# Kernel optimization log

Measured on AMD Instinct MI355X. Metric: run time of the kernel, lower is better.

The kernel has to match this reference:

```python
import jax, jax.numpy as jnp
import numpy as np

B, N, IN, HID, OUT = 64, 256, 7, 64, 32
DEG = 32
NT = B * N          # total nodes per side
E = NT * DEG        # intra-graph edges per side
TAU = 1.0
MAX_ITER = 10
EPS = 1e-5          # InstanceNorm2d eps


def setup_inputs() -> dict:
    key = jax.random.key(0)
    ks = jax.random.split(key, 12)

    def edges(k):
        # random intra-graph edges: local indices in [0, N) plus per-graph offset
        loc = jax.random.randint(k, (2, B, N * DEG), 0, N)
        off = (jnp.arange(B) * N)[None, :, None]
        return (loc + off).reshape(2, -1).astype(jnp.int64)

    def lin(k, fi, fo):
        return jax.random.normal(k, (fi, fo), jnp.float32) / np.float32(np.sqrt(fi))

    return {
        "x1": jax.random.normal(ks[0], (NT, IN), jnp.float32),
        "x2": jax.random.normal(ks[1], (NT, IN), jnp.float32),
        "edge1": edges(ks[2]),
        "edge2": edges(ks[3]),
        "Wl1": lin(ks[4], IN, HID), "Wr1": lin(ks[5], IN, HID),
        "bl1": jnp.zeros((HID,), jnp.float32), "br1": jnp.zeros((HID,), jnp.float32),
        "att1": jax.random.normal(ks[6], (HID,), jnp.float32) * 0.1,
        "bias1": jnp.zeros((HID,), jnp.float32),
        "Wl2": lin(ks[7], HID, OUT), "Wr2": lin(ks[8], HID, OUT),
        "bl2": jnp.zeros((OUT,), jnp.float32), "br2": jnp.zeros((OUT,), jnp.float32),
        "att2": jax.random.normal(ks[9], (OUT,), jnp.float32) * 0.1,
        "bias2": jnp.zeros((OUT,), jnp.float32),
        "gamma": jnp.ones((1,), jnp.float32),
        "beta": jnp.zeros((1,), jnp.float32),
    }


def _gatv2(x, src, dst, Wl, bl, Wr, br, att, bias):
    # PyG GATv2Conv, heads=1: score = att . leaky_relu(lin_l(x_j) + lin_r(x_i))
    xl = x @ Wl + bl  # source transform
    xr = x @ Wr + br  # target transform
    e = jax.nn.leaky_relu(xl[src] + xr[dst], 0.2)     # [E, D]
    score = e @ att                                    # [E]
    smax = jax.ops.segment_max(score, dst, num_segments=NT)
    ex = jnp.exp(score - smax[dst])
    den = jax.ops.segment_sum(ex, dst, num_segments=NT)
    alpha = ex / den[dst]
    out = jax.ops.segment_sum(alpha[:, None] * xl[src], dst, num_segments=NT)
    return out + bias


def _encode(x, edge, params):
    # add self loops (PyG add_self_loops=True default)
    loops = jnp.arange(NT)
    src = jnp.concatenate([edge[0], loops])
    dst = jnp.concatenate([edge[1], loops])
    h = jax.nn.relu(_gatv2(x, src, dst, *params[0]))
    return _gatv2(h, src, dst, *params[1])


def _soft_topk(sim_n):
    # AFAT-style differentiable top-k: OT between flattened scores and
    # {min, max} anchors with marginals [(n-k)/n, k/n], k = N2 per pair.
    n = N * N
    k = N
    flat = sim_n.reshape(B, n)
    mn = flat.min(axis=1, keepdims=True)
    mx = flat.max(axis=1, keepdims=True)
    dist = jnp.stack([flat - mn, mx - flat], axis=-1)  # [B, n, 2] (|s-min|,|s-max|)
    logK = -dist / TAU
    log_row = -jnp.log(jnp.float32(n))
    log_col = jnp.log(jnp.array([(n - k) / n, k / n], jnp.float32))
    for i in range(MAX_ITER):
        if i % 2 == 0:  # row normalization to uniform 1/n
            logK = logK - jax.scipy.special.logsumexp(logK, axis=-1, keepdims=True) + log_row
        else:           # column normalization to [(n-k)/n, k/n]
            logK = logK - jax.scipy.special.logsumexp(logK, axis=1, keepdims=True) + log_col[None, None, :]
    soft = jnp.clip(jnp.exp(logK[:, :, 1]) * n, 0.0, 1.0)  # selection probability per entry
    return soft.reshape(B, N, N)


def reference(x1, x2, edge1, edge2, Wl1, Wr1, bl1, br1, att1, bias1,
              Wl2, Wr2, bl2, br2, att2, bias2, gamma, beta):
    params = ((Wl1, bl1, Wr1, br1, att1, bias1), (Wl2, bl2, Wr2, br2, att2, bias2))
    h1 = _encode(x1, edge1, params).reshape(B, N, OUT)
    h2 = _encode(x2, edge2, params).reshape(B, N, OUT)
    sim = jnp.einsum('bnd,bmd->bnm', h1, h2)
    # InstanceNorm2d(1, affine=True): normalize each pair's sim matrix
    mu = sim.mean(axis=(1, 2), keepdims=True)
    var = sim.var(axis=(1, 2), keepdims=True)
    sim_n = gamma[0] * (sim - mu) * jax.lax.rsqrt(var + EPS) + beta[0]
    return _soft_topk(sim_n)  # soft_S stacked over the batch, [B, N, N]
```

## Files before the change

kernel.cpp:

```cpp
#include <hip/hip_runtime.h>

#define NB 64
#define NN 256
#define IND 7
#define HIDD 64
#define OUTD 32
#define EPG 8192
#define ETOT 524288
#define CAPQ 2600
#define SRCPAD 2624

typedef _Float16 f16;
typedef f16 f16x2 __attribute__((ext_vector_type(2)));
typedef f16 f16x4 __attribute__((ext_vector_type(4)));
typedef f16 f16x8 __attribute__((ext_vector_type(8)));
typedef float f32x4 __attribute__((ext_vector_type(4)));

__device__ __forceinline__ float bsum16(float v, float* rb){
#pragma unroll
  for (int o = 32; o > 0; o >>= 1) v += __shfl_xor(v, o, 64);
  __syncthreads();
  if ((threadIdx.x & 63) == 0) rb[threadIdx.x >> 6] = v;
  __syncthreads();
  float s = 0.f;
#pragma unroll
  for (int i = 0; i < 16; i++) s += rb[i];
  return s;
}

__device__ __forceinline__ f16x2 lrelu2(f16x2 s){
  const f16x2 k = {(f16)0.2f, (f16)0.2f};
  return __builtin_elementwise_max(s, s * k);
}
__device__ __forceinline__ f16x2 shfl_h2(f16x2 v, int lane){
  int i = __builtin_bit_cast(int, v);
  i = __shfl(i, lane, 64);
  return __builtin_bit_cast(f16x2, i);
}

__global__ __launch_bounds__(512, 4) void gat1(
    const float* __restrict__ x1, const float* __restrict__ x2,
    const int* __restrict__ e1, const int* __restrict__ e2,
    const float* __restrict__ Wl, const float* __restrict__ Wr,
    const float* __restrict__ bl, const float* __restrict__ br,
    const float* __restrict__ att, const float* __restrict__ bias,
    f16* __restrict__ hmid,
    int* __restrict__ meta, unsigned char* __restrict__ srcs)
{
  __shared__ __align__(16) f16 xl_s[256 * 72];
  __shared__ float sc_s[CAPQ + 8];
  __shared__ unsigned int src_su[SRCPAD / 4];
  __shared__ int deg_s[64], start_s[64], cnt_s[64];
  __shared__ unsigned char perm[64];
  unsigned char* src_s = (unsigned char*)src_su;

  const int bid = blockIdx.x;
  const int gs = bid & 127, lo = (bid >> 7) * 64;
  const int side = gs >> 6, g = gs & 63;
  const float* x = side ? x2 : x1;
  const int* eb = side ? e2 : e1;
  const int* es = eb + g * EPG;
  const int* ed = eb + ETOT + g * EPG;
  const int t = threadIdx.x;

  if (t < 64) deg_s[t] = 0;

  unsigned short epk[17];
  int nE = 0;
#pragma unroll
  for (int i = 0; i < 17; i++){
    int e = t + i * 512;
    if (e < EPG + 256){
      int sl, dl;
      if (e < EPG){ sl = es[e] & 255; dl = ed[e] & 255; }
      else { sl = dl = e - EPG; }
      epk[i] = (unsigned short)((dl << 8) | sl);
      nE = i + 1;
    }
  }

  {
    const int node = t >> 1, dh = t & 1;
    float xv[IND];
    const float* xr_ = x + (g * 256 + node) * IND;
#pragma unroll
    for (int k = 0; k < IND; k++) xv[k] = xr_[k];
#pragma unroll
    for (int ch = 0; ch < 4; ch++){
      f16x8 o;
#pragma unroll
      for (int j = 0; j < 8; j++){
        int dd = dh * 32 + ch * 8 + j;
        float a = bl[dd];
#pragma unroll
        for (int k = 0; k < IND; k++) a = fmaf(xv[k], Wl[k * HIDD + dd], a);
        o[j] = (f16)a;
      }
      *(f16x8*)&xl_s[node * 72 + dh * 32 + ch * 8] = o;
    }
  }
  __syncthreads();

#pragma unroll
  for (int i = 0; i < 17; i++) if (i < nE){
    int r = (epk[i] >> 8) - lo;
    if ((unsigned)r < 64u) atomicAdd(&deg_s[r], 1);
  }
  __syncthreads();
  if (t < 64){
    int v = deg_s[t], s = v;
#pragma unroll
    for (int off = 1; off < 64; off <<= 1){
      int u = __shfl_up(s, off, 64);
      if (t >= off) s += u;
    }
    start_s[t] = s - v;
    cnt_s[t] = s - v;
    meta[bid * 128 + t] = s - v;
    meta[bid * 128 + 64 + t] = v;
    int r = 0;
#pragma unroll 8
    for (int j = 0; j < 64; j++){
      int dj = deg_s[j];
      r += (dj < v) || (dj == v && j < t);
    }
    perm[r] = (unsigned char)t;
  }
  __syncthreads();
#pragma unroll
  for (int i = 0; i < 17; i++) if (i < nE){
    int dl = epk[i] >> 8, r = dl - lo;
    if ((unsigned)r < 64u){
      int p = atomicAdd(&cnt_s[r], 1);
      if (p < CAPQ) src_s[p] = (unsigned char)(epk[i] & 255);
    }
  }
  __syncthreads();
  {
    int ttl = start_s[63] + deg_s[63];
    if (ttl > CAPQ) ttl = CAPQ;
    unsigned int* gsrc = (unsigned int*)(srcs + (size_t)bid * SRCPAD);
    int nw = (ttl + 3) >> 2;
    for (int i = t; i < nw; i += 512) gsrc[i] = src_su[i];
  }

  const int pairi = perm[t >> 3], sub = t & 7, ln = lo + pairi;
  f16x2 m[4], am[4];
  {
    float xv[IND];
    const float* xq = x + (g * 256 + ln) * IND;
#pragma unroll
    for (int k = 0; k < IND; k++) xv[k] = xq[k];
#pragma unroll
    for (int c = 0; c < 4; c++){
#pragma unroll
      for (int u = 0; u < 2; u++){
        int dd = sub * 8 + 2 * c + u;
        float a = br[dd];
#pragma unroll
        for (int k = 0; k < IND; k++) a = fmaf(xv[k], Wr[k * HIDD + dd], a);
        m[c][u] = (f16)a;
        am[c][u] = (f16)att[dd];
      }
    }
  }
  f16x2 xrh[32], atth[32];
  {
    const int base = (t & 63) & ~7;
#pragma unroll
    for (int ss = 0; ss < 8; ss++){
#pragma unroll
      for (int c = 0; c < 4; c++){
        xrh[ss * 4 + c] = shfl_h2(m[c], base + ss);
        atth[ss * 4 + c] = shfl_h2(am[c], base + ss);
      }
    }
  }

  const int s0 = start_s[pairi];
  int sE = s0 + deg_s[pairi];
  if (sE > CAPQ) sE = CAPQ;
  float ssum = 0.f;
  for (int idx = s0 + sub; idx < sE; idx += 8){
    int sl = src_s[idx];
    const f16x8* rp = (const f16x8*)&xl_s[(unsigned)sl * 72];
    float accs[4] = {0.f, 0.f, 0.f, 0.f};
#pragma unroll
    for (int blk = 0; blk < 8; blk++){
      f16x8 rv = rp[blk];
#pragma unroll
      for (int u = 0; u < 4; u++){
        f16x2 v = {rv[2 * u], rv[2 * u + 1]};
        v = v + xrh[blk * 4 + u];
        accs[u] = __builtin_amdgcn_fdot2(lrelu2(v), atth[blk * 4 + u], accs[u], false);
      }
    }
    float w = __expf((accs[0] + accs[1]) + (accs[2] + accs[3]));
    sc_s[idx] = w;
    ssum += w;
  }
  ssum += __shfl_xor(ssum, 1, 64);
  ssum += __shfl_xor(ssum, 2, 64);
  ssum += __shfl_xor(ssum, 4, 64);
  float inv = 1.f / ssum;
  float acc[8];
#pragma unroll
  for (int c = 0; c < 8; c++) acc[c] = 0.f;
  for (int base = s0; base < sE; base += 4){
    f16x8 rows[4]; float wv[4];
#pragma unroll
    for (int k = 0; k < 4; k++){
      int sl = src_s[base + k];
      rows[k] = *(const f16x8*)&xl_s[(unsigned)sl * 72 + sub * 8];
      wv[k] = sc_s[base + k];
    }
#pragma unroll
    for (int k = 0; k < 4; k++){
      float w = (base + k < sE) ? wv[k] : 0.f;
#pragma unroll
      for (int c = 0; c < 8; c++) acc[c] = fmaf(w, (float)rows[k][c], acc[c]);
    }
  }
  f16x8 o;
#pragma unroll
  for (int c = 0; c < 8; c++)
    o[c] = (f16)fmaxf(acc[c] * inv + bias[sub * 8 + c], 0.f);
  *(f16x8*)(hmid + (size_t)(gs * 256 + ln) * 64 + sub * 8) = o;
}

__global__ __launch_bounds__(512, 4) void gat2(
    const int* __restrict__ meta, const unsigned char* __restrict__ srcs,
    const f16* __restrict__ hmid,
    const float* __restrict__ Wl, const float* __restrict__ Wr,
    const float* __restrict__ bl, const float* __restrict__ br,
    const float* __restrict__ att, const float* __restrict__ bias,
    f16* __restrict__ hout)
{
  __shared__ __align__(16) f16 xl_s[256 * 40];
  __shared__ __align__(16) f16 xr_s[64 * 40];
  __shared__ float sc_s[CAPQ + 8];
  __shared__ unsigned int src_su[SRCPAD / 4];
  __shared__ int start_s[64], deg_s[64];
  __shared__ unsigned char perm[64];
  unsigned char* src_s = (unsigned char*)src_su;

  const int bid = blockIdx.x;
  const int gs = bid & 127, lo = (bid >> 7) * 64;
  const int t = threadIdx.x;

  if (t < 64){
    start_s[t] = meta[bid * 128 + t];
    deg_s[t] = meta[bid * 128 + 64 + t];
  }
  {
    int ttl = meta[bid * 128 + 63] + meta[bid * 128 + 64 + 63];
    if (ttl > CAPQ) ttl = CAPQ;
    const unsigned int* gsrc = (const unsigned int*)(srcs + (size_t)bid * SRCPAD);
    int nw = (ttl + 3) >> 2;
    for (int i = t; i < nw; i += 512) src_su[i] = gsrc[i];
  }

  {
    const int w = t >> 6, lane = t & 63;
    const int m = lane & 15, quad = lane >> 4;
    f16x8 a[2][2];
#pragma unroll
    for (int ti = 0; ti < 2; ti++){
      const f16* arow = hmid + (size_t)(gs * 256 + (2 * w + ti) * 16 + m) * 64;
      a[ti][0] = *(const f16x8*)(arow + quad * 8);
      a[ti][1] = *(const f16x8*)(arow + 32 + quad * 8);
    }
#pragma unroll
    for (int H = 0; H < 2; H++){
      const int n = H * 16 + m;
      f16x8 b0, b1;
#pragma unroll
      for (int j = 0; j < 8; j++){
        b0[j] = (f16)Wl[(quad * 8 + j) * 32 + n];
        b1[j] = (f16)Wl[(32 + quad * 8 + j) * 32 + n];
      }
      const float bv = bl[n];
#pragma unroll
      for (int ti = 0; ti < 2; ti++){
        f32x4 acc = {0.f, 0.f, 0.f, 0.f};
        acc = __builtin_amdgcn_mfma_f32_16x16x32_f16(a[ti][0], b0, acc, 0, 0, 0);
        acc = __builtin_amdgcn_mfma_f32_16x16x32_f16(a[ti][1], b1, acc, 0, 0, 0);
#pragma unroll
        for (int r = 0; r < 4; r++)
          xl_s[((2 * w + ti) * 16 + quad * 4 + r) * 40 + n] = (f16)(acc[r] + bv);
      }
    }
    if (w < 4){
      const f16* arow = hmid + (size_t)(gs * 256 + lo + w * 16 + m) * 64;
      f16x8 c0 = *(const f16x8*)(arow + quad * 8);
      f16x8 c1 = *(const f16x8*)(arow + 32 + quad * 8);
#pragma unroll
      for (int H = 0; H < 2; H++){
        const int n = H * 16 + m;
        f16x8 b0, b1;
#pragma unroll
        for (int j = 0; j < 8; j++){
          b0[j] = (f16)Wr[(quad * 8 + j) * 32 + n];
          b1[j] = (f16)Wr[(32 + quad * 8 + j) * 32 + n];
        }
        const float bv = br[n];
        f32x4 acc = {0.f, 0.f, 0.f, 0.f};
        acc = __builtin_amdgcn_mfma_f32_16x16x32_f16(c0, b0, acc, 0, 0, 0);
        acc = __builtin_amdgcn_mfma_f32_16x16x32_f16(c1, b1, acc, 0, 0, 0);
#pragma unroll
        for (int r = 0; r < 4; r++)
          xr_s[(w * 16 + quad * 4 + r) * 40 + n] = (f16)(acc[r] + bv);
      }
    }
  }
  __syncthreads();
  if (t < 64){
    int v = deg_s[t], r = 0;
#pragma unroll 8
    for (int j = 0; j < 64; j++){
      int dj = deg_s[j];
      r += (dj < v) || (dj == v && j < t);
    }
    perm[r] = (unsigned char)t;
  }
  __syncthreads();

  const int pairi = perm[t >> 3], sub = t & 7, ln = lo + pairi;
  f16x2 xrh[16], atth[16];
  {
    const f16x8* xrp = (const f16x8*)&xr_s[pairi * 40];
#pragma unroll
    for (int q = 0; q < 4; q++){
      f16x8 v = xrp[q];
#pragma unroll
      for (int u = 0; u < 4; u++){
        xrh[q * 4 + u][0] = v[2 * u];
        xrh[q * 4 + u][1] = v[2 * u + 1];
      }
    }
#pragma unroll
    for (int i = 0; i < 16; i++){
      atth[i][0] = (f16)att[2 * i];
      atth[i][1] = (f16)att[2 * i + 1];
    }
  }

  const int s0 = start_s[pairi];
  int sE = s0 + deg_s[pairi];
  if (sE > CAPQ) sE = CAPQ;
  float ssum = 0.f;
  for (int idx = s0 + sub; idx < sE; idx += 8){
    int sl = src_s[idx];
    const f16x8* rp = (const f16x8*)&xl_s[(unsigned)sl * 40];
    float accs[4] = {0.f, 0.f, 0.f, 0.f};
#pragma unroll
    for (int blk = 0; blk < 4; blk++){
      f16x8 rv = rp[blk];
#pragma unroll
      for (int u = 0; u < 4; u++){
        f16x2 v = {rv[2 * u], rv[2 * u + 1]};
        v = v + xrh[blk * 4 + u];
        accs[u] = __builtin_amdgcn_fdot2(lrelu2(v), atth[blk * 4 + u], accs[u], false);
      }
    }
    float w = __expf((accs[0] + accs[1]) + (accs[2] + accs[3]));
    sc_s[idx] = w;
    ssum += w;
  }
  ssum += __shfl_xor(ssum, 1, 64);
  ssum += __shfl_xor(ssum, 2, 64);
  ssum += __shfl_xor(ssum, 4, 64);
  float inv = 1.f / ssum;

  float acc[4];
#pragma unroll
  for (int c = 0; c < 4; c++) acc[c] = 0.f;
  for (int base = s0; base < sE; base += 8){
    f16x4 rows[8]; float wv[8];
#pragma unroll
    for (int k = 0; k < 8; k++){
      int sl = src_s[base + k];
      rows[k] = *(const f16x4*)&xl_s[(unsigned)sl * 40 + sub * 4];
      wv[k] = sc_s[base + k];
    }
#pragma unroll
    for (int k = 0; k < 8; k++){
      float w = (base + k < sE) ? wv[k] : 0.f;
#pragma unroll
      for (int c = 0; c < 4; c++) acc[c] = fmaf(w, (float)rows[k][c], acc[c]);
    }
  }
  f16x4 o;
#pragma unroll
  for (int c = 0; c < 4; c++)
    o[c] = (f16)(acc[c] * inv + bias[sub * 4 + c]);
  *(f16x4*)(hout + (size_t)(gs * 256 + ln) * 32 + sub * 4) = o;
}

__global__ __launch_bounds__(1024) void sinkout(
    const f16* __restrict__ H,
    const float* __restrict__ gamma, const float* __restrict__ beta,
    float* __restrict__ out)
{
  __shared__ float rb[16];
  __shared__ __align__(16) float rb4s[64];
  __shared__ unsigned int hist[8192];
  const int b = blockIdx.x & 63, q = blockIdx.x >> 6, t = threadIdx.x;
  const int w = t >> 6, lane = t & 63;
  const int m = lane & 15, quad = lane >> 4;

  const f16* h1 = H + (size_t)b * 256 * 32;
  const f16* h2 = H + (size_t)(64 + b) * 256 * 32;

  f16x8 av = *(const f16x8*)(h1 + (size_t)(w * 16 + m) * 32 + quad * 8);
  f32x4 c[16];
#pragma unroll
  for (int j = 0; j < 16; j++){
    f16x8 bv = *(const f16x8*)(h2 + (size_t)(j * 16 + m) * 32 + quad * 8);
    f32x4 z = {0.f, 0.f, 0.f, 0.f};
    c[j] = __builtin_amdgcn_mfma_f32_16x16x32_f16(av, bv, z, 0, 0, 0);
  }

  float sm = 0.f, s2 = 0.f, mn = 3.0e38f, mx = -3.0e38f;
#pragma unroll
  for (int j = 0; j < 16; j++)
#pragma unroll
    for (int r = 0; r < 4; r++){
      float s = c[j][r];
      sm += s; s2 = fmaf(s, s, s2);
      mn = fminf(mn, s); mx = fmaxf(mx, s);
    }
#pragma unroll
  for (int o = 32; o > 0; o >>= 1){
    sm += __shfl_xor(sm, o, 64);
    s2 += __shfl_xor(s2, o, 64);
    mn = fminf(mn, __shfl_xor(mn, o, 64));
    mx = fmaxf(mx, __shfl_xor(mx, o, 64));
  }
  if (lane == 0){
    rb4s[w * 4 + 0] = sm; rb4s[w * 4 + 1] = s2;
    rb4s[w * 4 + 2] = mn; rb4s[w * 4 + 3] = mx;
  }
  for (int i = t; i < 8192; i += 1024) hist[i] = 0u;
  __syncthreads();
  sm = 0.f; s2 = 0.f; mn = 3.0e38f; mx = -3.0e38f;
#pragma unroll
  for (int i = 0; i < 16; i++){
    sm += rb4s[i * 4 + 0];
    s2 += rb4s[i * 4 + 1];
    mn = fminf(mn, rb4s[i * 4 + 2]);
    mx = fmaxf(mx, rb4s[i * 4 + 3]);
  }

  const float mu = sm * (1.f / 65536.f);
  const float var = s2 * (1.f / 65536.f) - mu * mu;
  const float a = gamma[0] * rsqrtf(var + 1e-5f);
  const float cc = beta[0] - a * mu;
  float mnn = a * mn + cc, mxn = a * mx + cc;
  if (a < 0.f){ float tmp = mnn; mnn = mxn; mxn = tmp; }
  const float al = 2.f * a;
  const float be = 2.f * cc - mnn - mxn;
  const float R = fmaxf(mxn - mnn, 1e-12f);
  const float binscale = 4096.f / R;

#pragma unroll
  for (int j = 0; j < 16; j++)
#pragma unroll
    for (int r = 0; r < 4; r++){
      float z = fmaf(al, c[j][r], be);
      int bi = (int)fmaf(z, binscale, 4096.f);
      bi = min(max(bi, 0), 8191);
      atomicAdd(&hist[bi], 1u);
    }
  __syncthreads();

  const float wbin = R * (1.f / 4096.f);
  float ebs[8], cnts[8];
#pragma unroll
  for (int j = 0; j < 8; j++){
    float zc = fmaf((float)(t * 8 + j) + 0.5f, wbin, -R);
    ebs[j] = __expf(-zc);
    cnts[j] = (float)hist[t * 8 + j];
  }

  float D = 0.f, S = 256.f, eD = 1.f;
  for (int p = 0; p < 5; p++){
    float loc = 0.f;
#pragma unroll
    for (int j = 0; j < 8; j++)
      loc += cnts[j] / (1.f + ebs[j] * eD);
    S = bsum16(loc, rb);
    if (p < 4){
      D += -5.5412635f  + __logf(65536.f - S) - __logf(S);
      eD = __expf(-D);
    }
  }

  const float beD = be + D;
  const float scale = 256.f / S;
  if ((w >> 2) == q){
    float* ob = out + (size_t)b * 65536;
#pragma unroll
    for (int j = 0; j < 16; j++){
#pragma unroll
      for (int r = 0; r < 4; r++){
        float zz = fmaf(al, c[j][r], beD);
        float v = fminf(scale / (1.f + __expf(-zz)), 1.f);
        ob[(w * 16 + quad * 4 + r) * 256 + j * 16 + m] = v;
      }
    }
  }
}

extern "C" void kernel_launch(void* const* d_in, const int* in_sizes, int n_in,
                              void* d_out, int out_size, void* d_ws, size_t ws_size,
                              hipStream_t stream)
{
  const float* x1   = (const float*)d_in[0];
  const float* x2   = (const float*)d_in[1];
  const int*   e1   = (const int*)d_in[2];
  const int*   e2   = (const int*)d_in[3];
  const float* Wl1  = (const float*)d_in[4];
  const float* Wr1  = (const float*)d_in[5];
  const float* bl1  = (const float*)d_in[6];
  const float* br1  = (const float*)d_in[7];
  const float* att1 = (const float*)d_in[8];
  const float* bias1= (const float*)d_in[9];
  const float* Wl2  = (const float*)d_in[10];
  const float* Wr2  = (const float*)d_in[11];
  const float* bl2  = (const float*)d_in[12];
  const float* br2  = (const float*)d_in[13];
  const float* att2 = (const float*)d_in[14];
  const float* bias2= (const float*)d_in[15];
  const float* gamma= (const float*)d_in[16];
  const float* beta = (const float*)d_in[17];

  char* ws = (char*)d_ws;
  f16* hfin = (f16*)ws;
  f16* hmid = (f16*)(ws + (size_t)2 * 1024 * 1024);
  int* meta = (int*)(ws + (size_t)6 * 1024 * 1024);
  unsigned char* srcs = (unsigned char*)(ws + (size_t)6 * 1024 * 1024 + 512 * 128 * 4);
  float* out = (float*)d_out;

  gat1<<<512, 512, 0, stream>>>(x1, x2, e1, e2, Wl1, Wr1, bl1, br1, att1, bias1,
                                hmid, meta, srcs);
  gat2<<<512, 512, 0, stream>>>(meta, srcs, hmid, Wl2, Wr2, bl2, br2, att2, bias2, hfin);
  sinkout<<<256, 1024, 0, stream>>>(hfin, gamma, beta, out);
}
```

Before: 169.1 us.

## Fuse layer-2 linear transforms into gat1 and stage layer-1 xr in shared memory

Each gat1 block now computes layer-2 xl/xr projections with MFMA for its 64 owned nodes and writes them to global memory, so gat2 only loads precomputed xl2/xr2 instead of recomputing xl for all 256 nodes per block (four times redundant). Layer-1 xr and att are computed once into shared memory instead of per-thread computation plus shuffle broadcasts, and the xl projection loop is restructured so weights are reused across 32 outputs. This adds extra shared memory and two barriers in gat1, which may affect occupancy.

```diff
diff --git a/kernel.cpp b/kernel.cpp
--- a/kernel.cpp
+++ b/kernel.cpp
@@ -32,11 +32,6 @@
   const f16x2 k = {(f16)0.2f, (f16)0.2f};
   return __builtin_elementwise_max(s, s * k);
 }
-__device__ __forceinline__ f16x2 shfl_h2(f16x2 v, int lane){
-  int i = __builtin_bit_cast(int, v);
-  i = __shfl(i, lane, 64);
-  return __builtin_bit_cast(f16x2, i);
-}
 
 __global__ __launch_bounds__(512, 4) void gat1(
     const float* __restrict__ x1, const float* __restrict__ x2,
@@ -44,10 +39,14 @@
     const float* __restrict__ Wl, const float* __restrict__ Wr,
     const float* __restrict__ bl, const float* __restrict__ br,
     const float* __restrict__ att, const float* __restrict__ bias,
-    f16* __restrict__ hmid,
+    const float* __restrict__ Wl2, const float* __restrict__ Wr2,
+    const float* __restrict__ bl2, const float* __restrict__ br2,
+    f16* __restrict__ xl2, f16* __restrict__ xr2,
     int* __restrict__ meta, unsigned char* __restrict__ srcs)
 {
   __shared__ __align__(16) f16 xl_s[256 * 72];
+  __shared__ __align__(16) f16 xr1_s[64 * 72];
+  __shared__ __align__(16) f16 att_s[64];
   __shared__ float sc_s[CAPQ + 8];
   __shared__ unsigned int src_su[SRCPAD / 4];
   __shared__ int deg_s[64], start_s[64], cnt_s[64];
@@ -62,8 +61,9 @@
   const int* es = eb + g * EPG;
   const int* ed = eb + ETOT + g * EPG;
   const int t = threadIdx.x;
-
-  if (t < 64) deg_s[t] = 0;
+  const int wv = t >> 6, lane64 = t & 63;
+
+  if (t < 64){ deg_s[t] = 0; att_s[t] = (f16)att[t]; }
 
   unsigned short epk[17];
   int nE = 0;
@@ -80,24 +80,51 @@
   }
 
   {
-    const int node = t >> 1, dh = t & 1;
+    const int ng = wv & 3, dh = wv >> 2;
+    const int node = ng * 64 + lane64;
     float xv[IND];
     const float* xr_ = x + (g * 256 + node) * IND;
 #pragma unroll
     for (int k = 0; k < IND; k++) xv[k] = xr_[k];
-#pragma unroll
-    for (int ch = 0; ch < 4; ch++){
+    float a[32];
+#pragma unroll
+    for (int d = 0; d < 32; d++) a[d] = bl[dh * 32 + d];
+#pragma unroll
+    for (int k = 0; k < IND; k++){
+      float xk = xv[k];
+#pragma unroll
+      for (int d = 0; d < 32; d++)
+        a[d] = fmaf(xk, Wl[k * HIDD + dh * 32 + d], a[d]);
+    }
+#pragma unroll
+    for (int c = 0; c < 4; c++){
       f16x8 o;
 #pragma unroll
-      for (int j = 0; j < 8; j++){
-        int dd = dh * 32 + ch * 8 + j;
-        float a = bl[dd];
-#pragma unroll
-        for (int k = 0; k < IND; k++) a = fmaf(xv[k], Wl[k * HIDD + dd], a);
-        o[j] = (f16)a;
-      }
-      *(f16x8*)&xl_s[node * 72 + dh * 32 + ch * 8] = o;
-    }
+      for (int j = 0; j < 8; j++) o[j] = (f16)a[c * 8 + j];
+      *(f16x8*)&xl_s[node * 72 + dh * 32 + c * 8] = o;
+    }
+  }
+  {
+    const int d0 = wv * 8;
+    const int node = lo + lane64;
+    float xv[IND];
+    const float* xq = x + (g * 256 + node) * IND;
+#pragma unroll
+    for (int k = 0; k < IND; k++) xv[k] = xq[k];
+    float a[8];
+#pragma unroll
+    for (int d = 0; d < 8; d++) a[d] = br[d0 + d];
+#pragma unroll
+    for (int k = 0; k < IND; k++){
+      float xk = xv[k];
+#pragma unroll
+      for (int d = 0; d < 8; d++)
+        a[d] = fmaf(xk, Wr[k * HIDD + d0 + d], a[d]);
+    }
+    f16x8 o;
+#pragma unroll
+    for (int j = 0; j < 8; j++) o[j] = (f16)a[j];
+    *(f16x8*)&xr1_s[lane64 * 72 + d0] = o;
   }
   __syncthreads();
 
@@ -145,36 +172,11 @@
   }
 
   const int pairi = perm[t >> 3], sub = t & 7, ln = lo + pairi;
-  f16x2 m[4], am[4];
-  {
-    float xv[IND];
-    const float* xq = x + (g * 256 + ln) * IND;
-#pragma unroll
-    for (int k = 0; k < IND; k++) xv[k] = xq[k];
-#pragma unroll
-    for (int c = 0; c < 4; c++){
-#pragma unroll
-      for (int u = 0; u < 2; u++){
-        int dd = sub * 8 + 2 * c + u;
-        float a = br[dd];
-#pragma unroll
-        for (int k = 0; k < IND; k++) a = fmaf(xv[k], Wr[k * HIDD + dd], a);
-        m[c][u] = (f16)a;
-        am[c][u] = (f16)att[dd];
-      }
-    }
-  }
-  f16x2 xrh[32], atth[32];
-  {
-    const int base = (t & 63) & ~7;
-#pragma unroll
-    for (int ss = 0; ss < 8; ss++){
-#pragma unroll
-      for (int c = 0; c < 4; c++){
-        xrh[ss * 4 + c] = shfl_h2(m[c], base + ss);
-        atth[ss * 4 + c] = shfl_h2(am[c], base + ss);
-      }
-    }
+  f16x8 xr8[8], at8[8];
+#pragma unroll
+  for (int q = 0; q < 8; q++){
+    xr8[q] = *(const f16x8*)&xr1_s[pairi * 72 + q * 8];
+    at8[q] = *(const f16x8*)&att_s[q * 8];
   }
 
   const int s0 = start_s[pairi];
@@ -188,11 +190,14 @@
 #pragma unroll
     for (int blk = 0; blk < 8; blk++){
       f16x8 rv = rp[blk];
+      f16x8 xb = xr8[blk], ab = at8[blk];
 #pragma unroll
       for (int u = 0; u < 4; u++){
         f16x2 v = {rv[2 * u], rv[2 * u + 1]};
-        v = v + xrh[blk * 4 + u];
-        accs[u] = __builtin_amdgcn_fdot2(lrelu2(v), atth[blk * 4 + u], accs[u], false);
+        f16x2 xx = {xb[2 * u], xb[2 * u + 1]};
+        f16x2 aa = {ab[2 * u], ab[2 * u + 1]};
+        v = v + xx;
+        accs[u] = __builtin_amdgcn_fdot2(lrelu2(v), aa, accs[u], false);
       }
     }
     float w = __expf((accs[0] + accs[1]) + (accs[2] + accs[3]));
@@ -207,16 +212,16 @@
 #pragma unroll
   for (int c = 0; c < 8; c++) acc[c] = 0.f;
   for (int base = s0; base < sE; base += 4){
-    f16x8 rows[4]; float wv[4];
+    f16x8 rows[4]; float wv_[4];
 #pragma unroll
     for (int k = 0; k < 4; k++){
       int sl = src_s[base + k];
       rows[k] = *(const f16x8*)&xl_s[(unsigned)sl * 72 + sub * 8];
-      wv[k] = sc_s[base + k];
+      wv_[k] = sc_s[base + k];
     }
 #pragma unroll
     for (int k = 0; k < 4; k++){
-      float w = (base + k < sE) ? wv[k] : 0.f;
+      float w = (base + k < sE) ? wv_[k] : 0.f;
 #pragma unroll
       for (int c = 0; c < 8; c++) acc[c] = fmaf(w, (float)rows[k][c], acc[c]);
     }
@@ -225,14 +230,45 @@
 #pragma unroll
   for (int c = 0; c < 8; c++)
     o[c] = (f16)fmaxf(acc[c] * inv + bias[sub * 8 + c], 0.f);
-  *(f16x8*)(hmid + (size_t)(gs * 256 + ln) * 64 + sub * 8) = o;
+
+  __syncthreads();
+  *(f16x8*)&xl_s[pairi * 72 + sub * 8] = o;
+  __syncthreads();
+  if (wv < 4){
+    const int m = lane64 & 15, quad = lane64 >> 4;
+    const int row = wv * 16 + m;
+    f16x8 a0 = *(const f16x8*)&xl_s[row * 72 + quad * 8];
+    f16x8 a1 = *(const f16x8*)&xl_s[row * 72 + 32 + quad * 8];
+#pragma unroll
+    for (int mat = 0; mat < 2; mat++){
+      const float* W = mat ? Wr2 : Wl2;
+      const float* bb = mat ? br2 : bl2;
+      f16* dst = mat ? xr2 : xl2;
+#pragma unroll
+      for (int H = 0; H < 2; H++){
+        const int n = H * 16 + m;
+        f16x8 b0, b1;
+#pragma unroll
+        for (int j = 0; j < 8; j++){
+          b0[j] = (f16)W[(quad * 8 + j) * 32 + n];
+          b1[j] = (f16)W[(32 + quad * 8 + j) * 32 + n];
+        }
+        const float bv = bb[n];
+        f32x4 accm = {0.f, 0.f, 0.f, 0.f};
+        accm = __builtin_amdgcn_mfma_f32_16x16x32_f16(a0, b0, accm, 0, 0, 0);
+        accm = __builtin_amdgcn_mfma_f32_16x16x32_f16(a1, b1, accm, 0, 0, 0);
+#pragma unroll
+        for (int r = 0; r < 4; r++)
+          dst[(size_t)(gs * 256 + lo + wv * 16 + quad * 4 + r) * 32 + n]
+              = (f16)(accm[r] + bv);
+      }
+    }
+  }
 }
 
 __global__ __launch_bounds__(512, 4) void gat2(
     const int* __restrict__ meta, const unsigned char* __restrict__ srcs,
-    const f16* __restrict__ hmid,
-    const float* __restrict__ Wl, const float* __restrict__ Wr,
-    const float* __restrict__ bl, const float* __restrict__ br,
+    const f16* __restrict__ xl2, const f16* __restrict__ xr2,
     const float* __restrict__ att, const float* __restrict__ bias,
     f16* __restrict__ hout)
 {
@@ -261,56 +297,14 @@
   }
 
   {
-    const int w = t >> 6, lane = t & 63;
-    const int m = lane & 15, quad = lane >> 4;
-    f16x8 a[2][2];
-#pragma unroll
-    for (int ti = 0; ti < 2; ti++){
-      const f16* arow = hmid + (size_t)(gs * 256 + (2 * w + ti) * 16 + m) * 64;
-      a[ti][0] = *(const f16x8*)(arow + quad * 8);
-      a[ti][1] = *(const f16x8*)(arow + 32 + quad * 8);
-    }
-#pragma unroll
-    for (int H = 0; H < 2; H++){
-      const int n = H * 16 + m;
-      f16x8 b0, b1;
-#pragma unroll
-      for (int j = 0; j < 8; j++){
-        b0[j] = (f16)Wl[(quad * 8 + j) * 32 + n];
-        b1[j] = (f16)Wl[(32 + quad * 8 + j) * 32 + n];
-      }
-      const float bv = bl[n];
-#pragma unroll
-      for (int ti = 0; ti < 2; ti++){
-        f32x4 acc = {0.f, 0.f, 0.f, 0.f};
-        acc = __builtin_amdgcn_mfma_f32_16x16x32_f16(a[ti][0], b0, acc, 0, 0, 0);
-        acc = __builtin_amdgcn_mfma_f32_16x16x32_f16(a[ti][1], b1, acc, 0, 0, 0);
-#pragma unroll
-        for (int r = 0; r < 4; r++)
-          xl_s[((2 * w + ti) * 16 + quad * 4 + r) * 40 + n] = (f16)(acc[r] + bv);
-      }
-    }
-    if (w < 4){
-      const f16* arow = hmid + (size_t)(gs * 256 + lo + w * 16 + m) * 64;
-      f16x8 c0 = *(const f16x8*)(arow + quad * 8);
-      f16x8 c1 = *(const f16x8*)(arow + 32 + quad * 8);
-#pragma unroll
-      for (int H = 0; H < 2; H++){
-        const int n = H * 16 + m;
-        f16x8 b0, b1;
-#pragma unroll
-        for (int j = 0; j < 8; j++){
-          b0[j] = (f16)Wr[(quad * 8 + j) * 32 + n];
-          b1[j] = (f16)Wr[(32 + quad * 8 + j) * 32 + n];
-        }
-        const float bv = br[n];
-        f32x4 acc = {0.f, 0.f, 0.f, 0.f};
-        acc = __builtin_amdgcn_mfma_f32_16x16x32_f16(c0, b0, acc, 0, 0, 0);
-        acc = __builtin_amdgcn_mfma_f32_16x16x32_f16(c1, b1, acc, 0, 0, 0);
-#pragma unroll
-        for (int r = 0; r < 4; r++)
-          xr_s[(w * 16 + quad * 4 + r) * 40 + n] = (f16)(acc[r] + bv);
-      }
+    const int row = t >> 1, half = t & 1;
+    const f16* s_ = xl2 + (size_t)(gs * 256 + row) * 32 + half * 16;
+    *(f16x8*)&xl_s[row * 40 + half * 16] = *(const f16x8*)s_;
+    *(f16x8*)&xl_s[row * 40 + half * 16 + 8] = *(const f16x8*)(s_ + 8);
+    if (t < 128){
+      const f16* s2_ = xr2 + (size_t)(gs * 256 + lo + row) * 32 + half * 16;
+      *(f16x8*)&xr_s[row * 40 + half * 16] = *(const f16x8*)s2_;
+      *(f16x8*)&xr_s[row * 40 + half * 16 + 8] = *(const f16x8*)(s2_ + 8);
     }
   }
   __syncthreads();
@@ -537,13 +531,14 @@
 
   char* ws = (char*)d_ws;
   f16* hfin = (f16*)ws;
-  f16* hmid = (f16*)(ws + (size_t)2 * 1024 * 1024);
+  f16* xl2 = (f16*)(ws + (size_t)2 * 1024 * 1024);
+  f16* xr2 = (f16*)(ws + (size_t)4 * 1024 * 1024);
   int* meta = (int*)(ws + (size_t)6 * 1024 * 1024);
   unsigned char* srcs = (unsigned char*)(ws + (size_t)6 * 1024 * 1024 + 512 * 128 * 4);
   float* out = (float*)d_out;
 
   gat1<<<512, 512, 0, stream>>>(x1, x2, e1, e2, Wl1, Wr1, bl1, br1, att1, bias1,
-                                hmid, meta, srcs);
-  gat2<<<512, 512, 0, stream>>>(meta, srcs, hmid, Wl2, Wr2, bl2, br2, att2, bias2, hfin);
+                                Wl2, Wr2, bl2, br2, xl2, xr2, meta, srcs);
+  gat2<<<512, 512, 0, stream>>>(meta, srcs, xl2, xr2, att2, bias2, hfin);
   sinkout<<<256, 1024, 0, stream>>>(hfin, gamma, beta, out);
 }
```

New measurement: 181.6 us. 7.4% more time.
